# Optimization experiments

Measured on AMD Instinct MI355X. Metric: run time of the kernel, lower is better.

## Reference

```python
import jax, jax.numpy as jnp
import numpy as np

B, L, D, H = 2, 1024, 1024, 16
HD = D // H
HIDDEN = 4 * D
EPS = 1e-6
SCALE = HD ** -0.5

# RoPE tables (head_dim is even, so rope_dim == head_dim)
_inv_freq = 1.0 / (10000.0 ** (np.arange(0, HD, 2, dtype=np.float32) / HD))
_freqs = np.arange(L, dtype=np.float32)[:, None] * _inv_freq[None, :]          # [L, HD/2]
COS = jnp.asarray(np.concatenate([np.cos(_freqs), np.cos(_freqs)], -1))        # [L, HD]
SIN = jnp.asarray(np.concatenate([np.sin(_freqs), np.sin(_freqs)], -1))
MASK = jnp.tril(jnp.ones((L, L), dtype=bool))                                   # causal


def _clin(xr, xi, Wr, Wi, br=None, bi=None):
    # complex linear: (a+bi)(c+di), weights stored [out, in] as in torch
    r = xr @ Wr.T - xi @ Wi.T
    i = xr @ Wi.T + xi @ Wr.T
    if br is not None:
        r = r + br
        i = i + bi
    return r, i


def _cln(xr, xi, gr, gi, br, bi):
    mr = xr.mean(-1, keepdims=True)
    mi = xi.mean(-1, keepdims=True)
    cr = xr - mr
    ci = xi - mi
    var = (cr * cr + ci * ci).mean(-1, keepdims=True)
    s = jnp.sqrt(var + EPS)
    nr = cr / s
    ni = ci / s
    return nr * gr - ni * gi + br, nr * gi + ni * gr + bi


def _rot_half(x):
    h = x.shape[-1] // 2
    return jnp.concatenate([-x[..., h:], x[..., :h]], -1)


def _rope(xr, xi):
    # apply same real rotation to real and imag parts (matches torch code)
    return (xr * COS + _rot_half(xr) * SIN, xi * COS + _rot_half(xi) * SIN)


def _split_heads(x):
    return x.reshape(B, L, H, HD).transpose(0, 2, 1, 3)  # [B,H,L,HD]


def _merge_heads(x):
    return x.transpose(0, 2, 1, 3).reshape(B, L, D)


def setup_inputs() -> dict:
    key = jax.random.key(0)
    ks = jax.random.split(key, 20)
    n = lambda k, shape, s=1.0: jax.random.normal(k, shape, dtype=jnp.float32) * s
    s_attn = (2.0 * (D + D)) ** -0.5
    s_fc1 = (2.0 * (D + HIDDEN)) ** -0.5
    s_fc2 = (2.0 * (HIDDEN + D)) ** -0.5
    return {
        'x_real': n(ks[0], (B, L, D)),
        'x_imag': n(ks[1], (B, L, D)),
        'Wq_r': n(ks[2], (D, D), s_attn), 'Wq_i': n(ks[3], (D, D), s_attn),
        'Wk_r': n(ks[4], (D, D), s_attn), 'Wk_i': n(ks[5], (D, D), s_attn),
        'Wv_r': n(ks[6], (D, D), s_attn), 'Wv_i': n(ks[7], (D, D), s_attn),
        'Wo_r': n(ks[8], (D, D), s_attn), 'Wo_i': n(ks[9], (D, D), s_attn),
        'bo_r': jnp.zeros((D,), jnp.float32), 'bo_i': jnp.zeros((D,), jnp.float32),
        'ln1_gr': jnp.ones((D,), jnp.float32), 'ln1_gi': jnp.zeros((D,), jnp.float32),
        'ln1_br': jnp.zeros((D,), jnp.float32), 'ln1_bi': jnp.zeros((D,), jnp.float32),
        'ln2_gr': jnp.ones((D,), jnp.float32), 'ln2_gi': jnp.zeros((D,), jnp.float32),
        'ln2_br': jnp.zeros((D,), jnp.float32), 'ln2_bi': jnp.zeros((D,), jnp.float32),
        'W1_r': n(ks[10], (HIDDEN, D), s_fc1), 'W1_i': n(ks[11], (HIDDEN, D), s_fc1),
        'b1_r': jnp.zeros((HIDDEN,), jnp.float32), 'b1_i': jnp.zeros((HIDDEN,), jnp.float32),
        'W2_r': n(ks[12], (D, HIDDEN), s_fc2), 'W2_i': n(ks[13], (D, HIDDEN), s_fc2),
        'b2_r': jnp.zeros((D,), jnp.float32), 'b2_i': jnp.zeros((D,), jnp.float32),
        'mod_b': n(ks[14], (HIDDEN,), 0.1),
    }


def reference(x_real, x_imag,
              Wq_r, Wq_i, Wk_r, Wk_i, Wv_r, Wv_i, Wo_r, Wo_i, bo_r, bo_i,
              ln1_gr, ln1_gi, ln1_br, ln1_bi, ln2_gr, ln2_gi, ln2_br, ln2_bi,
              W1_r, W1_i, b1_r, b1_i, W2_r, W2_i, b2_r, b2_i, mod_b):
    # --- attention sublayer (pre-LN) ---
    hr, hi = _cln(x_real, x_imag, ln1_gr, ln1_gi, ln1_br, ln1_bi)
    Qr, Qi = _clin(hr, hi, Wq_r, Wq_i)
    Kr, Ki = _clin(hr, hi, Wk_r, Wk_i)
    Vr, Vi = _clin(hr, hi, Wv_r, Wv_i)
    Qr, Qi, Kr, Ki = map(_split_heads, (Qr, Qi, Kr, Ki))
    Vr, Vi = _split_heads(Vr), _split_heads(Vi)
    Qr, Qi = _rope(Qr, Qi)
    Kr, Ki = _rope(Kr, Ki)
    # Hermitian inner product real part: Re(Q K*) = Qr.Kr + Qi.Ki
    scores = (jnp.einsum('bhld,bhmd->bhlm', Qr, Kr)
              + jnp.einsum('bhld,bhmd->bhlm', Qi, Ki)) * SCALE
    scores = jnp.where(MASK, scores, -jnp.inf)
    attn = jax.nn.softmax(scores, axis=-1)
    out_r = _merge_heads(jnp.einsum('bhlm,bhmd->bhld', attn, Vr))
    out_i = _merge_heads(jnp.einsum('bhlm,bhmd->bhld', attn, Vi))
    out_r, out_i = _clin(out_r, out_i, Wo_r, Wo_i, bo_r, bo_i)
    ar = x_real + out_r
    ai = x_imag + out_i
    # --- feed-forward sublayer (pre-LN) ---
    hr, hi = _cln(ar, ai, ln2_gr, ln2_gi, ln2_br, ln2_bi)
    fr, fi = _clin(hr, hi, W1_r, W1_i, b1_r, b1_i)
    # ModReLU: relu(|z| + b) * e^{i angle(z)}
    mag = jnp.sqrt(fr * fr + fi * fi)
    safe = jnp.where(mag > 0, mag, 1.0)
    act = jax.nn.relu(mag + mod_b)
    fr, fi = act * fr / safe, act * fi / safe
    fr, fi = _clin(fr, fi, W2_r, W2_i, b2_r, b2_i)
    return ar + fr, ai + fi
```

## Files before the change

### kernel.cpp

```cpp
#include <hip/hip_runtime.h>

#define Bq 2
#define Lq 1024
#define Dq 1024
#define Hq 16
#define HDq 64
#define HIDq 4096
#define Mq (Bq*Lq)

typedef __bf16 bf16x8 __attribute__((ext_vector_type(8)));
typedef float floatx4 __attribute__((ext_vector_type(4)));
typedef float floatx16 __attribute__((ext_vector_type(16)));

__device__ __forceinline__ unsigned short f2us(float f){
  unsigned u = __builtin_bit_cast(unsigned, f);
  u = u + 0x7fffu + ((u >> 16) & 1u);
  return (unsigned short)(u >> 16);
}

__device__ __forceinline__ void gld16(const unsigned short* g, unsigned short* l){
  __builtin_amdgcn_global_load_lds(
      (const __attribute__((address_space(1))) unsigned int*)g,
      (__attribute__((address_space(3))) unsigned int*)l, 16, 0, 0);
}

__global__ __launch_bounds__(256) void cvt4_kernel(
    const float* __restrict__ s0, const float* __restrict__ s1,
    const float* __restrict__ s2, const float* __restrict__ s3,
    unsigned short* __restrict__ d0, unsigned short* __restrict__ d1,
    unsigned short* __restrict__ d2, unsigned short* __restrict__ d3,
    int n)
{
  const int a = blockIdx.y;
  const float* s = (a==0) ? s0 : (a==1) ? s1 : (a==2) ? s2 : s3;
  unsigned short* d = (a==0) ? d0 : (a==1) ? d1 : (a==2) ? d2 : d3;
  const int i = (blockIdx.x * 256 + threadIdx.x) * 8;
  if (i >= n) return;
  float4 v0 = ((const float4*)(s + i))[0];
  float4 v1 = ((const float4*)(s + i))[1];
  ushort4 o0, o1;
  o0.x=f2us(v0.x); o0.y=f2us(v0.y); o0.z=f2us(v0.z); o0.w=f2us(v0.w);
  o1.x=f2us(v1.x); o1.y=f2us(v1.y); o1.z=f2us(v1.z); o1.w=f2us(v1.w);
  ((ushort4*)(d + i))[0] = o0;
  ((ushort4*)(d + i))[1] = o1;
}

__global__ __launch_bounds__(256) void cln_kernel(
    const float* __restrict__ xr, const float* __restrict__ xi,
    const float* __restrict__ gr, const float* __restrict__ gi,
    const float* __restrict__ br, const float* __restrict__ bi,
    unsigned short* __restrict__ outr, unsigned short* __restrict__ outi)
{
  const int row = blockIdx.x;
  const int t = threadIdx.x;
  const int lane = t & 63, wv = t >> 6;
  __shared__ float sred[8];

  float4 v4r = ((const float4*)(xr + (size_t)row*Dq))[t];
  float4 v4i = ((const float4*)(xi + (size_t)row*Dq))[t];
  float vr[4] = {v4r.x, v4r.y, v4r.z, v4r.w};
  float vi[4] = {v4i.x, v4i.y, v4i.z, v4i.w};
  float sr = vr[0]+vr[1]+vr[2]+vr[3];
  float si = vi[0]+vi[1]+vi[2]+vi[3];
  #pragma unroll
  for (int o=32;o>0;o>>=1){ sr += __shfl_down(sr,o,64); si += __shfl_down(si,o,64); }
  if (lane==0){ sred[wv]=sr; sred[4+wv]=si; }
  __syncthreads();
  float mr = (sred[0]+sred[1]+sred[2]+sred[3]) * (1.0f/Dq);
  float mi = (sred[4]+sred[5]+sred[6]+sred[7]) * (1.0f/Dq);
  float cr[4], ci[4], vs = 0.f;
  #pragma unroll
  for (int j=0;j<4;++j){ cr[j]=vr[j]-mr; ci[j]=vi[j]-mi; vs += cr[j]*cr[j]+ci[j]*ci[j]; }
  #pragma unroll
  for (int o=32;o>0;o>>=1) vs += __shfl_down(vs,o,64);
  __syncthreads();
  if (lane==0) sred[wv]=vs;
  __syncthreads();
  float var = (sred[0]+sred[1]+sred[2]+sred[3]) * (1.0f/Dq);
  float inv = rsqrtf(var + 1e-6f);

  float4 g4r = ((const float4*)gr)[t];
  float4 g4i = ((const float4*)gi)[t];
  float4 b4r = ((const float4*)br)[t];
  float4 b4i = ((const float4*)bi)[t];
  float grf[4] = {g4r.x,g4r.y,g4r.z,g4r.w};
  float gif[4] = {g4i.x,g4i.y,g4i.z,g4i.w};
  float brf[4] = {b4r.x,b4r.y,b4r.z,b4r.w};
  float bif[4] = {b4i.x,b4i.y,b4i.z,b4i.w};
  ushort4 o_r, o_i;
  unsigned short orr[4], oii[4];
  #pragma unroll
  for (int j=0;j<4;++j){
    float nr = cr[j]*inv, ni = ci[j]*inv;
    orr[j] = f2us(nr*grf[j] - ni*gif[j] + brf[j]);
    oii[j] = f2us(nr*gif[j] + ni*grf[j] + bif[j]);
  }
  o_r.x=orr[0]; o_r.y=orr[1]; o_r.z=orr[2]; o_r.w=orr[3];
  o_i.x=oii[0]; o_i.y=oii[1]; o_i.z=oii[2]; o_i.w=oii[3];
  ((ushort4*)(outr + (size_t)row*Dq))[t] = o_r;
  ((ushort4*)(outi + (size_t)row*Dq))[t] = o_i;
}

template<int EPI, bool ROPE, bool SPLIT3>
__global__ __launch_bounds__(128,2) void cgemm32_kernel(
    const unsigned short* __restrict__ Ar, const unsigned short* __restrict__ Ai,
    const unsigned short* __restrict__ Wr, const unsigned short* __restrict__ Wi,
    void* __restrict__ Cr0, void* __restrict__ Ci0,
    void* __restrict__ Cr1, void* __restrict__ Ci1,
    void* __restrict__ Cr2, void* __restrict__ Ci2,
    const float* __restrict__ biasR, const float* __restrict__ biasI,
    const float* __restrict__ resR, const float* __restrict__ resI,
    const float* __restrict__ modb,
    int Ndim, int Kdim)
{
  const int t = threadIdx.x;
  const int w = t >> 6, l = t & 63;
  const int l31 = l & 31, lhi = l >> 5;
  const int m0 = blockIdx.x * 64, n0 = blockIdx.y * 64;

  __shared__ __align__(16) unsigned short sAr0[64*64], sAi0[64*64], sWr0[64*64], sWi0[64*64];
  __shared__ __align__(16) unsigned short sAr1[64*64], sAi1[64*64], sWr1[64*64], sWi1[64*64];

  floatx16 accRR[2], accII[2], accRI[2], accIR[2];
  #pragma unroll
  for (int i=0;i<2;++i){
    #pragma unroll
    for (int r=0;r<16;++r){ accRR[i][r]=0.f; accII[i][r]=0.f; accRI[i][r]=0.f; accIR[i][r]=0.f; }
  }

  const int srow = t >> 3;
  const int lc = (((t & 7) ^ ((t >> 3) & 7))) * 8;
  const unsigned short* pAr = Ar + (size_t)(m0 + srow)*Kdim + lc;
  const unsigned short* pAi = Ai + (size_t)(m0 + srow)*Kdim + lc;
  const unsigned short* pWr = Wr + (size_t)(n0 + srow)*Kdim + lc;
  const unsigned short* pWi = Wi + (size_t)(n0 + srow)*Kdim + lc;
  const int dst0 = t * 8;

  const int arow = w*32 + l31;
  int aoff[4], woff0[4], woff1[4];
  #pragma unroll
  for (int kh=0; kh<4; ++kh){
    const int c = kh*2 + lhi;
    aoff[kh]  = arow*64      + ((c ^ (arow & 7)) * 8);
    woff0[kh] = l31*64       + ((c ^ (l31 & 7)) * 8);
    woff1[kh] = (32+l31)*64  + ((c ^ (l31 & 7)) * 8);
  }

#define STAGEK(SA, SB, SC, SD, KOFF) do{                                   \
    _Pragma("unroll")                                                      \
    for (int j_=0;j_<4;++j_){                                              \
      const size_t so_ = (size_t)j_ * 16 * Kdim + (size_t)(KOFF);          \
      gld16(pAr + so_, &SA[dst0 + j_*1024]);                               \
      gld16(pAi + so_, &SB[dst0 + j_*1024]);                               \
      gld16(pWr + so_, &SC[dst0 + j_*1024]);                               \
      gld16(pWi + so_, &SD[dst0 + j_*1024]);                               \
    } }while(0)

#define COMPUTEK(SA, SB, SC, SD) do{                                       \
    _Pragma("unroll")                                                      \
    for (int kh_=0; kh_<4; ++kh_){                                         \
      bf16x8 fAr  = *(const bf16x8*)&SA[aoff[kh_]];                        \
      bf16x8 fAi  = *(const bf16x8*)&SB[aoff[kh_]];                        \
      bf16x8 fW0r = *(const bf16x8*)&SC[woff0[kh_]];                       \
      bf16x8 fW0i = *(const bf16x8*)&SD[woff0[kh_]];                       \
      bf16x8 fW1r = *(const bf16x8*)&SC[woff1[kh_]];                       \
      bf16x8 fW1i = *(const bf16x8*)&SD[woff1[kh_]];                       \
      accRR[0] = __builtin_amdgcn_mfma_f32_32x32x16_bf16(fAr, fW0r, accRR[0], 0,0,0); \
      accII[0] = __builtin_amdgcn_mfma_f32_32x32x16_bf16(fAi, fW0i, accII[0], 0,0,0); \
      accRI[0] = __builtin_amdgcn_mfma_f32_32x32x16_bf16(fAr, fW0i, accRI[0], 0,0,0); \
      accIR[0] = __builtin_amdgcn_mfma_f32_32x32x16_bf16(fAi, fW0r, accIR[0], 0,0,0); \
      accRR[1] = __builtin_amdgcn_mfma_f32_32x32x16_bf16(fAr, fW1r, accRR[1], 0,0,0); \
      accII[1] = __builtin_amdgcn_mfma_f32_32x32x16_bf16(fAi, fW1i, accII[1], 0,0,0); \
      accRI[1] = __builtin_amdgcn_mfma_f32_32x32x16_bf16(fAr, fW1i, accRI[1], 0,0,0); \
      accIR[1] = __builtin_amdgcn_mfma_f32_32x32x16_bf16(fAi, fW1r, accIR[1], 0,0,0); \
    } }while(0)

  const int nk = Kdim >> 6;
  STAGEK(sAr0, sAi0, sWr0, sWi0, 0);
  __syncthreads();
  for (int kk=0; kk<nk; kk+=2){
    STAGEK(sAr1, sAi1, sWr1, sWi1, (kk+1)*64);
    COMPUTEK(sAr0, sAi0, sWr0, sWi0);
    __syncthreads();
    if (kk+2 < nk) STAGEK(sAr0, sAi0, sWr0, sWi0, (kk+2)*64);
    COMPUTEK(sAr1, sAi1, sWr1, sWi1);
    __syncthreads();
  }
#undef STAGEK
#undef COMPUTEK

  float cr[2][16], ci[2][16];
  #pragma unroll
  for (int nf=0; nf<2; ++nf)
    #pragma unroll
    for (int r=0;r<16;++r){
      cr[nf][r] = accRR[nf][r] - accII[nf][r];
      ci[nf][r] = accRI[nf][r] + accIR[nf][r];
    }

  const bool doRope = ROPE && (!SPLIT3 || (n0 < 2048));
  if (doRope){
    const float invf = powf(10000.0f, -(float)l31 * (1.0f/32.0f));
    #pragma unroll
    for (int r=0;r<16;++r){
      const int gm = m0 + w*32 + (r&3) + 8*(r>>2) + 4*lhi;
      float s, c;
      sincosf((float)(gm & (Lq-1)) * invf, &s, &c);
      float xr_ = cr[0][r], yr_ = cr[1][r];
      cr[0][r] = xr_*c - yr_*s;  cr[1][r] = yr_*c + xr_*s;
      float xi_ = ci[0][r], yi_ = ci[1][r];
      ci[0][r] = xi_*c - yi_*s;  ci[1][r] = yi_*c + xi_*s;
    }
  }

  unsigned short *oR16 = nullptr, *oI16 = nullptr;
  float *oR32 = nullptr, *oI32 = nullptr;
  int ncol0, Nst;
  if (SPLIT3){
    const int aid = n0 >> 10;
    void* vr = (aid==0) ? Cr0 : ((aid==1) ? Cr1 : Cr2);
    void* vi = (aid==0) ? Ci0 : ((aid==1) ? Ci1 : Ci2);
    oR16 = (unsigned short*)vr; oI16 = (unsigned short*)vi;
    ncol0 = n0 & 1023; Nst = 1024;
  } else {
    oR16 = (unsigned short*)Cr0; oI16 = (unsigned short*)Ci0;
    oR32 = (float*)Cr0;          oI32 = (float*)Ci0;
    ncol0 = n0; Nst = Ndim;
  }

  #pragma unroll
  for (int nf=0; nf<2; ++nf){
    const int gn = n0 + nf*32 + l31;
    const int cn = ncol0 + nf*32 + l31;
    float bR = 0.f, bI = 0.f, mb = 0.f;
    if (EPI >= 1){ bR = biasR[gn]; bI = biasI[gn]; }
    if (EPI == 2){ mb = modb[gn]; }
    #pragma unroll
    for (int r=0;r<16;++r){
      const int gm = m0 + w*32 + (r&3) + 8*(r>>2) + 4*lhi;
      const size_t idx = (size_t)gm*Nst + cn;
      float vr_ = cr[nf][r] + bR, vi_ = ci[nf][r] + bI;
      if (EPI == 1 || EPI == 3){ vr_ += resR[idx]; vi_ += resI[idx]; }
      if (EPI == 2){
        float mag = sqrtf(vr_*vr_ + vi_*vi_);
        float safe = (mag > 0.f) ? mag : 1.0f;
        float act = fmaxf(mag + mb, 0.f);
        float sc = act / safe;
        vr_ *= sc; vi_ *= sc;
      }
      if (EPI == 0 || EPI == 2){
        oR16[idx] = f2us(vr_);
        oI16[idx] = f2us(vi_);
      } else {
        oR32[idx] = vr_;
        oI32[idx] = vi_;
      }
    }
  }
}

__global__ __launch_bounds__(256) void vtrans_kernel(
    const unsigned short* __restrict__ Vr, const unsigned short* __restrict__ Vi,
    unsigned short* __restrict__ VTr, unsigned short* __restrict__ VTi)
{
  const int lt = blockIdx.x;
  const int bh = blockIdx.y;
  const int h = bh & (Hq-1), b = bh >> 4;
  const int t = threadIdx.x;
  __shared__ unsigned short sTr[64*65], sTi[64*65];

  const int row = t >> 2;
  const int dc  = (t & 3) * 16;
  const size_t g = ((size_t)(b*Lq) + lt*64 + row)*Dq + h*HDq + dc;
  uint4 a0 = *(const uint4*)(Vr + g);
  uint4 a1 = *(const uint4*)(Vr + g + 8);
  uint4 b0 = *(const uint4*)(Vi + g);
  uint4 b1 = *(const uint4*)(Vi + g + 8);
  const unsigned short* pa0 = (const unsigned short*)&a0;
  const unsigned short* pa1 = (const unsigned short*)&a1;
  const unsigned short* pb0 = (const unsigned short*)&b0;
  const unsigned short* pb1 = (const unsigned short*)&b1;
  #pragma unroll
  for (int e=0;e<8;++e){
    sTr[(dc+e)*65 + row]   = pa0[e];
    sTr[(dc+8+e)*65 + row] = pa1[e];
    sTi[(dc+e)*65 + row]   = pb0[e];
    sTi[(dc+8+e)*65 + row] = pb1[e];
  }
  __syncthreads();
  const int d  = t >> 2;
  const int lcx = (t & 3) * 16;
  unsigned short bufr[16], bufi[16];
  #pragma unroll
  for (int e=0;e<16;++e){
    bufr[e] = sTr[d*65 + lcx + e];
    bufi[e] = sTi[d*65 + lcx + e];
  }
  const size_t og = ((size_t)bh*HDq + d)*Lq + lt*64 + lcx;
  *(uint4*)(VTr + og)     = *(const uint4*)&bufr[0];
  *(uint4*)(VTr + og + 8) = *(const uint4*)&bufr[8];
  *(uint4*)(VTi + og)     = *(const uint4*)&bufi[0];
  *(uint4*)(VTi + og + 8) = *(const uint4*)&bufi[8];
}

__device__ __forceinline__ int swz(int v){ return v ^ ((v >> 4) & 7); }

__global__ __launch_bounds__(256,2) void fattn_kernel(
    const unsigned short* __restrict__ Qr, const unsigned short* __restrict__ Qi,
    const unsigned short* __restrict__ Kr, const unsigned short* __restrict__ Ki,
    const unsigned short* __restrict__ VTr, const unsigned short* __restrict__ VTi,
    unsigned short* __restrict__ Or, unsigned short* __restrict__ Oi)
{
  const int qt = (int)(gridDim.x - 1 - blockIdx.x);
  const int bh = blockIdx.y;
  const int h = bh & (Hq-1), b = bh >> 4;
  const int t = threadIdx.x;
  const int w = t >> 6, lane = t & 63;
  const int quad = lane >> 4, l15 = lane & 15;

  __shared__ __align__(16) unsigned short sKr[4096], sKi[4096], sVr[4096], sVi[4096];
  __shared__ __align__(16) unsigned short sP[64*72];

  const size_t qbase = ((size_t)(b*Lq) + qt*64 + w*16 + l15)*Dq + h*HDq;
  bf16x8 qr_lo = *(const bf16x8*)(Qr + qbase + quad*8);
  bf16x8 qr_hi = *(const bf16x8*)(Qr + qbase + 32 + quad*8);
  bf16x8 qi_lo = *(const bf16x8*)(Qi + qbase + quad*8);
  bf16x8 qi_hi = *(const bf16x8*)(Qi + qbase + 32 + quad*8);

  const floatx4 fzero = {0.f,0.f,0.f,0.f};
  floatx4 aOr[4], aOi[4];
  #pragma unroll
  for (int i=0;i<4;++i){ aOr[i]=fzero; aOi[i]=fzero; }
  float m_run[4] = {-1e30f,-1e30f,-1e30f,-1e30f};
  float l_run[4] = {0.f,0.f,0.f,0.f};

  const int srow = t >> 2;
  const int sns  = srow >> 4;
  const int sl15 = srow & 15;
  const int q8   = (t & 3) * 2;
  const int dstA = sns*1024 + swz(q8*16 + sl15)*8;
  const int dstB = sns*1024 + swz((q8+1)*16 + sl15)*8;

  const int rd0 = swz(quad*16 + l15)*8;
  const int rd1 = swz((4+quad)*16 + l15)*8;

  for (int kt = 0; kt <= qt; ++kt){
    const size_t kg = ((size_t)(b*Lq) + kt*64 + srow)*Dq + h*HDq + q8*8;
    uint4 ka = *(const uint4*)(Kr + kg);
    uint4 kb = *(const uint4*)(Kr + kg + 8);
    uint4 kc = *(const uint4*)(Ki + kg);
    uint4 kd = *(const uint4*)(Ki + kg + 8);
    const size_t vg = ((size_t)bh*HDq + srow)*Lq + kt*64 + q8*8;
    uint4 va = *(const uint4*)(VTr + vg);
    uint4 vb = *(const uint4*)(VTr + vg + 8);
    uint4 vc = *(const uint4*)(VTi + vg);
    uint4 vd = *(const uint4*)(VTi + vg + 8);
    __syncthreads();
    *(uint4*)&sKr[dstA] = ka;  *(uint4*)&sKr[dstB] = kb;
    *(uint4*)&sKi[dstA] = kc;  *(uint4*)&sKi[dstB] = kd;
    *(uint4*)&sVr[dstA] = va;  *(uint4*)&sVr[dstB] = vb;
    *(uint4*)&sVi[dstA] = vc;  *(uint4*)&sVi[dstB] = vd;
    __syncthreads();

    floatx4 sc[4];
    #pragma unroll
    for (int ns=0; ns<4; ++ns){
      floatx4 x = fzero;
      x = __builtin_amdgcn_mfma_f32_16x16x32_bf16(qr_lo, *(const bf16x8*)&sKr[ns*1024 + rd0], x, 0,0,0);
      x = __builtin_amdgcn_mfma_f32_16x16x32_bf16(qr_hi, *(const bf16x8*)&sKr[ns*1024 + rd1], x, 0,0,0);
      x = __builtin_amdgcn_mfma_f32_16x16x32_bf16(qi_lo, *(const bf16x8*)&sKi[ns*1024 + rd0], x, 0,0,0);
      x = __builtin_amdgcn_mfma_f32_16x16x32_bf16(qi_hi, *(const bf16x8*)&sKi[ns*1024 + rd1], x, 0,0,0);
      sc[ns] = x;
    }

    const bool diag = (kt == qt);
    float rmax[4] = {-1e30f,-1e30f,-1e30f,-1e30f};
    #pragma unroll
    for (int ns=0; ns<4; ++ns){
      #pragma unroll
      for (int r=0; r<4; ++r){
        float s = sc[ns][r] * 0.125f;
        if (diag && (ns*16 + l15 > w*16 + quad*4 + r)) s = -1e30f;
        sc[ns][r] = s;
        rmax[r] = fmaxf(rmax[r], s);
      }
    }
    #pragma unroll
    for (int off=1; off<16; off<<=1){
      #pragma unroll
      for (int r=0; r<4; ++r) rmax[r] = fmaxf(rmax[r], __shfl_xor(rmax[r], off, 64));
    }

    float alpha[4], rsum[4];
    #pragma unroll
    for (int r=0; r<4; ++r){
      float mn = fmaxf(m_run[r], rmax[r]);
      alpha[r] = __expf(m_run[r] - mn);
      m_run[r] = mn;
      rsum[r] = 0.f;
    }
    #pragma unroll
    for (int ns=0; ns<4; ++ns){
      #pragma unroll
      for (int r=0; r<4; ++r){
        float p = __expf(sc[ns][r] - m_run[r]);
        rsum[r] += p;
        sP[(w*16 + quad*4 + r)*72 + ns*16 + l15] = f2us(p);
      }
    }
    #pragma unroll
    for (int off=1; off<16; off<<=1){
      #pragma unroll
      for (int r=0; r<4; ++r) rsum[r] += __shfl_xor(rsum[r], off, 64);
    }
    #pragma unroll
    for (int r=0; r<4; ++r) l_run[r] = l_run[r]*alpha[r] + rsum[r];
    #pragma unroll
    for (int ds=0; ds<4; ++ds)
      #pragma unroll
      for (int r=0; r<4; ++r){ aOr[ds][r] *= alpha[r]; aOi[ds][r] *= alpha[r]; }

    #pragma unroll
    for (int step=0; step<2; ++step){
      bf16x8 pf = *(const bf16x8*)&sP[(w*16 + l15)*72 + step*32 + quad*8];
      const int ro = (step==0) ? rd0 : rd1;
      #pragma unroll
      for (int ds=0; ds<4; ++ds){
        aOr[ds] = __builtin_amdgcn_mfma_f32_16x16x32_bf16(pf, *(const bf16x8*)&sVr[ds*1024 + ro], aOr[ds], 0,0,0);
        aOi[ds] = __builtin_amdgcn_mfma_f32_16x16x32_bf16(pf, *(const bf16x8*)&sVi[ds*1024 + ro], aOi[ds], 0,0,0);
      }
    }
  }

  #pragma unroll
  for (int r=0; r<4; ++r){
    const float il = 1.0f / l_run[r];
    const size_t ob = ((size_t)(b*Lq) + qt*64 + w*16 + quad*4 + r)*Dq + h*HDq;
    #pragma unroll
    for (int ds=0; ds<4; ++ds){
      Or[ob + ds*16 + l15] = f2us(aOr[ds][r] * il);
      Oi[ob + ds*16 + l15] = f2us(aOi[ds][r] * il);
    }
  }
}

extern "C" void kernel_launch(void* const* d_in, const int* in_sizes, int n_in,
                              void* d_out, int out_size, void* d_ws, size_t ws_size,
                              hipStream_t stream)
{
  const float* x_r    = (const float*)d_in[0];
  const float* x_i    = (const float*)d_in[1];
  const float* Wq_r   = (const float*)d_in[2];
  const float* Wq_i   = (const float*)d_in[3];
  const float* Wk_r   = (const float*)d_in[4];
  const float* Wk_i   = (const float*)d_in[5];
  const float* Wv_r   = (const float*)d_in[6];
  const float* Wv_i   = (const float*)d_in[7];
  const float* Wo_r   = (const float*)d_in[8];
  const float* Wo_i   = (const float*)d_in[9];
  const float* bo_r   = (const float*)d_in[10];
  const float* bo_i   = (const float*)d_in[11];
  const float* ln1_gr = (const float*)d_in[12];
  const float* ln1_gi = (const float*)d_in[13];
  const float* ln1_br = (const float*)d_in[14];
  const float* ln1_bi = (const float*)d_in[15];
  const float* ln2_gr = (const float*)d_in[16];
  const float* ln2_gi = (const float*)d_in[17];
  const float* ln2_br = (const float*)d_in[18];
  const float* ln2_bi = (const float*)d_in[19];
  const float* W1_r   = (const float*)d_in[20];
  const float* W1_i   = (const float*)d_in[21];
  const float* b1_r   = (const float*)d_in[22];
  const float* b1_i   = (const float*)d_in[23];
  const float* W2_r   = (const float*)d_in[24];
  const float* W2_i   = (const float*)d_in[25];
  const float* b2_r   = (const float*)d_in[26];
  const float* b2_i   = (const float*)d_in[27];
  const float* mod_b  = (const float*)d_in[28];

  char* wsb = (char*)d_ws;
  const size_t MB = 1024*1024;
  unsigned short* bQKV_r = (unsigned short*)(wsb + 0*MB);
  unsigned short* bQKV_i = (unsigned short*)(wsb + 6*MB);
  unsigned short* bWo_r = (unsigned short*)(wsb + 12*MB);
  unsigned short* bWo_i = (unsigned short*)(wsb + 14*MB);
  unsigned short* bW1_r = (unsigned short*)(wsb + 16*MB);
  unsigned short* bW1_i = (unsigned short*)(wsb + 24*MB);
  unsigned short* bW2_r = (unsigned short*)(wsb + 32*MB);
  unsigned short* bW2_i = (unsigned short*)(wsb + 40*MB);
  unsigned short* hr  = (unsigned short*)(wsb + 48*MB);
  unsigned short* hi_ = (unsigned short*)(wsb + 52*MB);
  unsigned short* Qr  = (unsigned short*)(wsb + 56*MB);
  unsigned short* Qi  = (unsigned short*)(wsb + 60*MB);
  unsigned short* Kr  = (unsigned short*)(wsb + 64*MB);
  unsigned short* Ki  = (unsigned short*)(wsb + 68*MB);
  unsigned short* Vr  = (unsigned short*)(wsb + 72*MB);
  unsigned short* Vi  = (unsigned short*)(wsb + 76*MB);
  unsigned short* VTr = (unsigned short*)(wsb + 80*MB);
  unsigned short* VTi = (unsigned short*)(wsb + 84*MB);
  unsigned short* Or  = hr;
  unsigned short* Oi  = hi_;
  unsigned short* h2r = Qr;
  unsigned short* h2i = Qi;
  unsigned short* fr  = (unsigned short*)(wsb + 64*MB);
  unsigned short* fi  = (unsigned short*)(wsb + 80*MB);

  float* outR = (float*)d_out;
  float* outI = outR + (size_t)Mq*Dq;

  const dim3 blk(256);
  const dim3 blk128(128);

  const int nDD = Dq*Dq;
  const int nDH = Dq*HIDq;
  cvt4_kernel<<<dim3(nDD/2048, 4), blk, 0, stream>>>(Wq_r, Wk_r, Wv_r, Wo_r,
      bQKV_r, bQKV_r + (size_t)nDD, bQKV_r + (size_t)2*nDD, bWo_r, nDD);
  cvt4_kernel<<<dim3(nDD/2048, 4), blk, 0, stream>>>(Wq_i, Wk_i, Wv_i, Wo_i,
      bQKV_i, bQKV_i + (size_t)nDD, bQKV_i + (size_t)2*nDD, bWo_i, nDD);
  cvt4_kernel<<<dim3(nDH/2048, 4), blk, 0, stream>>>(W1_r, W1_i, W2_r, W2_i,
      bW1_r, bW1_i, bW2_r, bW2_i, nDH);

  cln_kernel<<<Mq, blk, 0, stream>>>(x_r, x_i, ln1_gr, ln1_gi, ln1_br, ln1_bi, hr, hi_);
  cgemm32_kernel<0,true,true><<<dim3(Mq/64, 3072/64), blk128, 0, stream>>>(
      hr, hi_, bQKV_r, bQKV_i,
      Qr, Qi, Kr, Ki, Vr, Vi,
      nullptr, nullptr, nullptr, nullptr, nullptr, 3072, Dq);
  vtrans_kernel<<<dim3(16, 32), blk, 0, stream>>>(Vr, Vi, VTr, VTi);
  fattn_kernel<<<dim3(16, 32), blk, 0, stream>>>(Qr, Qi, Kr, Ki, VTr, VTi, Or, Oi);
  cgemm32_kernel<1,false,false><<<dim3(Mq/64, Dq/64), blk128, 0, stream>>>(
      Or, Oi, bWo_r, bWo_i, outR, outI, nullptr, nullptr, nullptr, nullptr,
      bo_r, bo_i, x_r, x_i, nullptr, Dq, Dq);
  cln_kernel<<<Mq, blk, 0, stream>>>(outR, outI, ln2_gr, ln2_gi, ln2_br, ln2_bi, h2r, h2i);
  cgemm32_kernel<2,false,false><<<dim3(Mq/64, HIDq/64), blk128, 0, stream>>>(
      h2r, h2i, bW1_r, bW1_i, fr, fi, nullptr, nullptr, nullptr, nullptr,
      b1_r, b1_i, nullptr, nullptr, mod_b, HIDq, Dq);
  cgemm32_kernel<3,false,false><<<dim3(Mq/64, Dq/64), blk128, 0, stream>>>(
      fr, fi, bW2_r, bW2_i, outR, outI, nullptr, nullptr, nullptr, nullptr,
      b2_r, b2_i, outR, outI, nullptr, Dq, HIDq);
}
```

Measured before the change: 507.1 us.

## Switch complex GEMM to 16x16x32 MFMA with 4 waves and BK=32

Rewrites the complex GEMM kernel to use 256 threads (4 waves in a 2x2 grid) with 16x16x32 bf16 MFMA tiles instead of 2 waves with 32x32x16 MFMA, and halves the K-step staged into LDS to 32. The LDS footprint drops and the launch bound rises to allow more resident blocks, aiming at better latency hiding and occupancy. The trade-off is more sync barriers per K and less operand reuse per wave, since each wave covers a 32x32 output tile instead of 32x64. RoPE and epilogue indexing are remapped to the new accumulator layout.

```diff
diff --git a/kernel.cpp b/kernel.cpp
--- a/kernel.cpp
+++ b/kernel.cpp
@@ -10,7 +10,6 @@
 
 typedef __bf16 bf16x8 __attribute__((ext_vector_type(8)));
 typedef float floatx4 __attribute__((ext_vector_type(4)));
-typedef float floatx16 __attribute__((ext_vector_type(16)));
 
 __device__ __forceinline__ unsigned short f2us(float f){
   unsigned u = __builtin_bit_cast(unsigned, f);
@@ -102,7 +101,7 @@
 }
 
 template<int EPI, bool ROPE, bool SPLIT3>
-__global__ __launch_bounds__(128,2) void cgemm32_kernel(
+__global__ __launch_bounds__(256,3) void cgemm16_kernel(
     const unsigned short* __restrict__ Ar, const unsigned short* __restrict__ Ai,
     const unsigned short* __restrict__ Wr, const unsigned short* __restrict__ Wi,
     void* __restrict__ Cr0, void* __restrict__ Ci0,
@@ -114,103 +113,110 @@
     int Ndim, int Kdim)
 {
   const int t = threadIdx.x;
-  const int w = t >> 6, l = t & 63;
-  const int l31 = l & 31, lhi = l >> 5;
+  const int w = t >> 6, lane = t & 63;
+  const int quad = lane >> 4, l15 = lane & 15;
+  const int wr = w >> 1, wc = w & 1;
   const int m0 = blockIdx.x * 64, n0 = blockIdx.y * 64;
 
-  __shared__ __align__(16) unsigned short sAr0[64*64], sAi0[64*64], sWr0[64*64], sWi0[64*64];
-  __shared__ __align__(16) unsigned short sAr1[64*64], sAi1[64*64], sWr1[64*64], sWi1[64*64];
-
-  floatx16 accRR[2], accII[2], accRI[2], accIR[2];
-  #pragma unroll
-  for (int i=0;i<2;++i){
-    #pragma unroll
-    for (int r=0;r<16;++r){ accRR[i][r]=0.f; accII[i][r]=0.f; accRI[i][r]=0.f; accIR[i][r]=0.f; }
-  }
-
-  const int srow = t >> 3;
-  const int lc = (((t & 7) ^ ((t >> 3) & 7))) * 8;
+  __shared__ __align__(16) unsigned short sAr0[64*32], sAi0[64*32], sWr0[64*32], sWi0[64*32];
+  __shared__ __align__(16) unsigned short sAr1[64*32], sAi1[64*32], sWr1[64*32], sWi1[64*32];
+
+  const floatx4 fz = {0.f,0.f,0.f,0.f};
+  floatx4 accRR[2][2], accII[2][2], accRI[2][2], accIR[2][2];
+  #pragma unroll
+  for (int i=0;i<2;++i)
+    #pragma unroll
+    for (int j=0;j<2;++j){ accRR[i][j]=fz; accII[i][j]=fz; accRI[i][j]=fz; accIR[i][j]=fz; }
+
+  const int srow = t >> 2;
+  const int lc = ((t & 3) ^ ((t >> 2) & 3)) * 8;
   const unsigned short* pAr = Ar + (size_t)(m0 + srow)*Kdim + lc;
   const unsigned short* pAi = Ai + (size_t)(m0 + srow)*Kdim + lc;
   const unsigned short* pWr = Wr + (size_t)(n0 + srow)*Kdim + lc;
   const unsigned short* pWi = Wi + (size_t)(n0 + srow)*Kdim + lc;
   const int dst0 = t * 8;
 
-  const int arow = w*32 + l31;
-  int aoff[4], woff0[4], woff1[4];
-  #pragma unroll
-  for (int kh=0; kh<4; ++kh){
-    const int c = kh*2 + lhi;
-    aoff[kh]  = arow*64      + ((c ^ (arow & 7)) * 8);
-    woff0[kh] = l31*64       + ((c ^ (l31 & 7)) * 8);
-    woff1[kh] = (32+l31)*64  + ((c ^ (l31 & 7)) * 8);
-  }
+  const int arow0 = wr*32 + l15,       arow1 = arow0 + 16;
+  const int wrow0 = wc*16 + l15,       wrow1 = wrow0 + 32;
+  const int aoff0 = arow0*32 + ((quad ^ (arow0 & 3))*8);
+  const int aoff1 = arow1*32 + ((quad ^ (arow1 & 3))*8);
+  const int woff0 = wrow0*32 + ((quad ^ (wrow0 & 3))*8);
+  const int woff1 = wrow1*32 + ((quad ^ (wrow1 & 3))*8);
 
 #define STAGEK(SA, SB, SC, SD, KOFF) do{                                   \
-    _Pragma("unroll")                                                      \
-    for (int j_=0;j_<4;++j_){                                              \
-      const size_t so_ = (size_t)j_ * 16 * Kdim + (size_t)(KOFF);          \
-      gld16(pAr + so_, &SA[dst0 + j_*1024]);                               \
-      gld16(pAi + so_, &SB[dst0 + j_*1024]);                               \
-      gld16(pWr + so_, &SC[dst0 + j_*1024]);                               \
-      gld16(pWi + so_, &SD[dst0 + j_*1024]);                               \
-    } }while(0)
+    gld16(pAr + (KOFF), &SA[dst0]);                                        \
+    gld16(pAi + (KOFF), &SB[dst0]);                                        \
+    gld16(pWr + (KOFF), &SC[dst0]);                                        \
+    gld16(pWi + (KOFF), &SD[dst0]);                                        \
+  }while(0)
 
 #define COMPUTEK(SA, SB, SC, SD) do{                                       \
-    _Pragma("unroll")                                                      \
-    for (int kh_=0; kh_<4; ++kh_){                                         \
-      bf16x8 fAr  = *(const bf16x8*)&SA[aoff[kh_]];                        \
-      bf16x8 fAi  = *(const bf16x8*)&SB[aoff[kh_]];                        \
-      bf16x8 fW0r = *(const bf16x8*)&SC[woff0[kh_]];                       \
-      bf16x8 fW0i = *(const bf16x8*)&SD[woff0[kh_]];                       \
-      bf16x8 fW1r = *(const bf16x8*)&SC[woff1[kh_]];                       \
-      bf16x8 fW1i = *(const bf16x8*)&SD[woff1[kh_]];                       \
-      accRR[0] = __builtin_amdgcn_mfma_f32_32x32x16_bf16(fAr, fW0r, accRR[0], 0,0,0); \
-      accII[0] = __builtin_amdgcn_mfma_f32_32x32x16_bf16(fAi, fW0i, accII[0], 0,0,0); \
-      accRI[0] = __builtin_amdgcn_mfma_f32_32x32x16_bf16(fAr, fW0i, accRI[0], 0,0,0); \
-      accIR[0] = __builtin_amdgcn_mfma_f32_32x32x16_bf16(fAi, fW0r, accIR[0], 0,0,0); \
-      accRR[1] = __builtin_amdgcn_mfma_f32_32x32x16_bf16(fAr, fW1r, accRR[1], 0,0,0); \
-      accII[1] = __builtin_amdgcn_mfma_f32_32x32x16_bf16(fAi, fW1i, accII[1], 0,0,0); \
-      accRI[1] = __builtin_amdgcn_mfma_f32_32x32x16_bf16(fAr, fW1i, accRI[1], 0,0,0); \
-      accIR[1] = __builtin_amdgcn_mfma_f32_32x32x16_bf16(fAi, fW1r, accIR[1], 0,0,0); \
-    } }while(0)
-
-  const int nk = Kdim >> 6;
+    bf16x8 fA0r = *(const bf16x8*)&SA[aoff0];                              \
+    bf16x8 fA1r = *(const bf16x8*)&SA[aoff1];                              \
+    bf16x8 fA0i = *(const bf16x8*)&SB[aoff0];                              \
+    bf16x8 fA1i = *(const bf16x8*)&SB[aoff1];                              \
+    bf16x8 fW0r = *(const bf16x8*)&SC[woff0];                              \
+    bf16x8 fW1r = *(const bf16x8*)&SC[woff1];                              \
+    bf16x8 fW0i = *(const bf16x8*)&SD[woff0];                              \
+    bf16x8 fW1i = *(const bf16x8*)&SD[woff1];                              \
+    accRR[0][0] = __builtin_amdgcn_mfma_f32_16x16x32_bf16(fA0r, fW0r, accRR[0][0], 0,0,0); \
+    accII[0][0] = __builtin_amdgcn_mfma_f32_16x16x32_bf16(fA0i, fW0i, accII[0][0], 0,0,0); \
+    accRI[0][0] = __builtin_amdgcn_mfma_f32_16x16x32_bf16(fA0r, fW0i, accRI[0][0], 0,0,0); \
+    accIR[0][0] = __builtin_amdgcn_mfma_f32_16x16x32_bf16(fA0i, fW0r, accIR[0][0], 0,0,0); \
+    accRR[0][1] = __builtin_amdgcn_mfma_f32_16x16x32_bf16(fA0r, fW1r, accRR[0][1], 0,0,0); \
+    accII[0][1] = __builtin_amdgcn_mfma_f32_16x16x32_bf16(fA0i, fW1i, accII[0][1], 0,0,0); \
+    accRI[0][1] = __builtin_amdgcn_mfma_f32_16x16x32_bf16(fA0r, fW1i, accRI[0][1], 0,0,0); \
+    accIR[0][1] = __builtin_amdgcn_mfma_f32_16x16x32_bf16(fA0i, fW1r, accIR[0][1], 0,0,0); \
+    accRR[1][0] = __builtin_amdgcn_mfma_f32_16x16x32_bf16(fA1r, fW0r, accRR[1][0], 0,0,0); \
+    accII[1][0] = __builtin_amdgcn_mfma_f32_16x16x32_bf16(fA1i, fW0i, accII[1][0], 0,0,0); \
+    accRI[1][0] = __builtin_amdgcn_mfma_f32_16x16x32_bf16(fA1r, fW0i, accRI[1][0], 0,0,0); \
+    accIR[1][0] = __builtin_amdgcn_mfma_f32_16x16x32_bf16(fA1i, fW0r, accIR[1][0], 0,0,0); \
+    accRR[1][1] = __builtin_amdgcn_mfma_f32_16x16x32_bf16(fA1r, fW1r, accRR[1][1], 0,0,0); \
+    accII[1][1] = __builtin_amdgcn_mfma_f32_16x16x32_bf16(fA1i, fW1i, accII[1][1], 0,0,0); \
+    accRI[1][1] = __builtin_amdgcn_mfma_f32_16x16x32_bf16(fA1r, fW1i, accRI[1][1], 0,0,0); \
+    accIR[1][1] = __builtin_amdgcn_mfma_f32_16x16x32_bf16(fA1i, fW1r, accIR[1][1], 0,0,0); \
+  }while(0)
+
+  const int nk = Kdim >> 5;
   STAGEK(sAr0, sAi0, sWr0, sWi0, 0);
   __syncthreads();
   for (int kk=0; kk<nk; kk+=2){
-    STAGEK(sAr1, sAi1, sWr1, sWi1, (kk+1)*64);
+    STAGEK(sAr1, sAi1, sWr1, sWi1, (size_t)(kk+1)*32);
     COMPUTEK(sAr0, sAi0, sWr0, sWi0);
     __syncthreads();
-    if (kk+2 < nk) STAGEK(sAr0, sAi0, sWr0, sWi0, (kk+2)*64);
+    if (kk+2 < nk) STAGEK(sAr0, sAi0, sWr0, sWi0, (size_t)(kk+2)*32);
     COMPUTEK(sAr1, sAi1, sWr1, sWi1);
     __syncthreads();
   }
 #undef STAGEK
 #undef COMPUTEK
 
-  float cr[2][16], ci[2][16];
-  #pragma unroll
-  for (int nf=0; nf<2; ++nf)
-    #pragma unroll
-    for (int r=0;r<16;++r){
-      cr[nf][r] = accRR[nf][r] - accII[nf][r];
-      ci[nf][r] = accRI[nf][r] + accIR[nf][r];
-    }
+  float cr[2][2][4], ci[2][2][4];
+  #pragma unroll
+  for (int mf=0; mf<2; ++mf)
+    #pragma unroll
+    for (int nf=0; nf<2; ++nf)
+      #pragma unroll
+      for (int r=0;r<4;++r){
+        cr[mf][nf][r] = accRR[mf][nf][r] - accII[mf][nf][r];
+        ci[mf][nf][r] = accRI[mf][nf][r] + accIR[mf][nf][r];
+      }
 
   const bool doRope = ROPE && (!SPLIT3 || (n0 < 2048));
   if (doRope){
-    const float invf = powf(10000.0f, -(float)l31 * (1.0f/32.0f));
-    #pragma unroll
-    for (int r=0;r<16;++r){
-      const int gm = m0 + w*32 + (r&3) + 8*(r>>2) + 4*lhi;
-      float s, c;
-      sincosf((float)(gm & (Lq-1)) * invf, &s, &c);
-      float xr_ = cr[0][r], yr_ = cr[1][r];
-      cr[0][r] = xr_*c - yr_*s;  cr[1][r] = yr_*c + xr_*s;
-      float xi_ = ci[0][r], yi_ = ci[1][r];
-      ci[0][r] = xi_*c - yi_*s;  ci[1][r] = yi_*c + xi_*s;
-    }
+    const float invf = powf(10000.0f, -(float)(wc*16 + l15) * (1.0f/32.0f));
+    #pragma unroll
+    for (int mf=0; mf<2; ++mf)
+      #pragma unroll
+      for (int r=0;r<4;++r){
+        const int gm = m0 + wr*32 + mf*16 + quad*4 + r;
+        float s, c;
+        sincosf((float)(gm & (Lq-1)) * invf, &s, &c);
+        float xr_ = cr[mf][0][r], yr_ = cr[mf][1][r];
+        cr[mf][0][r] = xr_*c - yr_*s;  cr[mf][1][r] = yr_*c + xr_*s;
+        float xi_ = ci[mf][0][r], yi_ = ci[mf][1][r];
+        ci[mf][0][r] = xi_*c - yi_*s;  ci[mf][1][r] = yi_*c + xi_*s;
+      }
   }
 
   unsigned short *oR16 = nullptr, *oI16 = nullptr;
@@ -230,32 +236,34 @@
 
   #pragma unroll
   for (int nf=0; nf<2; ++nf){
-    const int gn = n0 + nf*32 + l31;
-    const int cn = ncol0 + nf*32 + l31;
+    const int gn = n0 + wc*16 + nf*32 + l15;
+    const int cn = ncol0 + wc*16 + nf*32 + l15;
     float bR = 0.f, bI = 0.f, mb = 0.f;
     if (EPI >= 1){ bR = biasR[gn]; bI = biasI[gn]; }
     if (EPI == 2){ mb = modb[gn]; }
     #pragma unroll
-    for (int r=0;r<16;++r){
-      const int gm = m0 + w*32 + (r&3) + 8*(r>>2) + 4*lhi;
-      const size_t idx = (size_t)gm*Nst + cn;
-      float vr_ = cr[nf][r] + bR, vi_ = ci[nf][r] + bI;
-      if (EPI == 1 || EPI == 3){ vr_ += resR[idx]; vi_ += resI[idx]; }
-      if (EPI == 2){
-        float mag = sqrtf(vr_*vr_ + vi_*vi_);
-        float safe = (mag > 0.f) ? mag : 1.0f;
-        float act = fmaxf(mag + mb, 0.f);
-        float sc = act / safe;
-        vr_ *= sc; vi_ *= sc;
+    for (int mf=0; mf<2; ++mf)
+      #pragma unroll
+      for (int r=0;r<4;++r){
+        const int gm = m0 + wr*32 + mf*16 + quad*4 + r;
+        const size_t idx = (size_t)gm*Nst + cn;
+        float vr_ = cr[mf][nf][r] + bR, vi_ = ci[mf][nf][r] + bI;
+        if (EPI == 1 || EPI == 3){ vr_ += resR[idx]; vi_ += resI[idx]; }
+        if (EPI == 2){
+          float mag = sqrtf(vr_*vr_ + vi_*vi_);
+          float safe = (mag > 0.f) ? mag : 1.0f;
+          float act = fmaxf(mag + mb, 0.f);
+          float sc = act / safe;
+          vr_ *= sc; vi_ *= sc;
+        }
+        if (EPI == 0 || EPI == 2){
+          oR16[idx] = f2us(vr_);
+          oI16[idx] = f2us(vi_);
+        } else {
+          oR32[idx] = vr_;
+          oI32[idx] = vi_;
+        }
       }
-      if (EPI == 0 || EPI == 2){
-        oR16[idx] = f2us(vr_);
-        oI16[idx] = f2us(vi_);
-      } else {
-        oR32[idx] = vr_;
-        oI32[idx] = vi_;
-      }
-    }
   }
 }
 
@@ -509,7 +517,6 @@
   float* outI = outR + (size_t)Mq*Dq;
 
   const dim3 blk(256);
-  const dim3 blk128(128);
 
   const int nDD = Dq*Dq;
   const int nDH = Dq*HIDq;
@@ -521,20 +528,20 @@
       bW1_r, bW1_i, bW2_r, bW2_i, nDH);
 
   cln_kernel<<<Mq, blk, 0, stream>>>(x_r, x_i, ln1_gr, ln1_gi, ln1_br, ln1_bi, hr, hi_);
-  cgemm32_kernel<0,true,true><<<dim3(Mq/64, 3072/64), blk128, 0, stream>>>(
+  cgemm16_kernel<0,true,true><<<dim3(Mq/64, 3072/64), blk, 0, stream>>>(
       hr, hi_, bQKV_r, bQKV_i,
       Qr, Qi, Kr, Ki, Vr, Vi,
       nullptr, nullptr, nullptr, nullptr, nullptr, 3072, Dq);
   vtrans_kernel<<<dim3(16, 32), blk, 0, stream>>>(Vr, Vi, VTr, VTi);
   fattn_kernel<<<dim3(16, 32), blk, 0, stream>>>(Qr, Qi, Kr, Ki, VTr, VTi, Or, Oi);
-  cgemm32_kernel<1,false,false><<<dim3(Mq/64, Dq/64), blk128, 0, stream>>>(
+  cgemm16_kernel<1,false,false><<<dim3(Mq/64, Dq/64), blk, 0, stream>>>(
       Or, Oi, bWo_r, bWo_i, outR, outI, nullptr, nullptr, nullptr, nullptr,
       bo_r, bo_i, x_r, x_i, nullptr, Dq, Dq);
   cln_kernel<<<Mq, blk, 0, stream>>>(outR, outI, ln2_gr, ln2_gi, ln2_br, ln2_bi, h2r, h2i);
-  cgemm32_kernel<2,false,false><<<dim3(Mq/64, HIDq/64), blk128, 0, stream>>>(
+  cgemm16_kernel<2,false,false><<<dim3(Mq/64, HIDq/64), blk, 0, stream>>>(
       h2r, h2i, bW1_r, bW1_i, fr, fi, nullptr, nullptr, nullptr, nullptr,
       b1_r, b1_i, nullptr, nullptr, mod_b, HIDq, Dq);
-  cgemm32_kernel<3,false,false><<<dim3(Mq/64, Dq/64), blk128, 0, stream>>>(
+  cgemm16_kernel<3,false,false><<<dim3(Mq/64, Dq/64), blk, 0, stream>>>(
       fr, fi, bW2_r, bW2_i, outR, outI, nullptr, nullptr, nullptr, nullptr,
       b2_r, b2_i, outR, outI, nullptr, Dq, HIDq);
 }
```

After: 522.4 us. +3.0%, slower.

## Widen complex GEMM tile to 64x128 with four waves and K-step 32

Applied to the files above, without the earlier changes.

The complex GEMM block grows from 128 threads on a 64x64 output tile to 256 threads on a 64x128 tile. Each wave is placed on a 2x2 grid inside the block, and the K step per stage shrinks from 64 to 32. The shared-memory layout packs two rows per 64-element line with a new XOR swizzle. The goal is more A-tile reuse across N and more waves per block for latency hiding, at the cost of twice as many barriers per K and half as many blocks in each grid.

```diff
diff --git a/kernel.cpp b/kernel.cpp
--- a/kernel.cpp
+++ b/kernel.cpp
@@ -102,7 +102,7 @@
 }
 
 template<int EPI, bool ROPE, bool SPLIT3>
-__global__ __launch_bounds__(128,2) void cgemm32_kernel(
+__global__ __launch_bounds__(256,2) void cgemm_kernel(
     const unsigned short* __restrict__ Ar, const unsigned short* __restrict__ Ai,
     const unsigned short* __restrict__ Wr, const unsigned short* __restrict__ Wi,
     void* __restrict__ Cr0, void* __restrict__ Ci0,
@@ -116,10 +116,11 @@
   const int t = threadIdx.x;
   const int w = t >> 6, l = t & 63;
   const int l31 = l & 31, lhi = l >> 5;
-  const int m0 = blockIdx.x * 64, n0 = blockIdx.y * 64;
-
-  __shared__ __align__(16) unsigned short sAr0[64*64], sAi0[64*64], sWr0[64*64], sWi0[64*64];
-  __shared__ __align__(16) unsigned short sAr1[64*64], sAi1[64*64], sWr1[64*64], sWi1[64*64];
+  const int wm = w >> 1, wn = w & 1;
+  const int m0 = blockIdx.x * 64, n0 = blockIdx.y * 128;
+
+  __shared__ __align__(16) unsigned short sAr0[2048], sAi0[2048], sWr0[4096], sWi0[4096];
+  __shared__ __align__(16) unsigned short sAr1[2048], sAi1[2048], sWr1[4096], sWi1[4096];
 
   floatx16 accRR[2], accII[2], accRI[2], accIR[2];
   #pragma unroll
@@ -128,43 +129,53 @@
     for (int r=0;r<16;++r){ accRR[i][r]=0.f; accII[i][r]=0.f; accRI[i][r]=0.f; accIR[i][r]=0.f; }
   }
 
-  const int srow = t >> 3;
-  const int lc = (((t & 7) ^ ((t >> 3) & 7))) * 8;
-  const unsigned short* pAr = Ar + (size_t)(m0 + srow)*Kdim + lc;
-  const unsigned short* pAi = Ai + (size_t)(m0 + srow)*Kdim + lc;
-  const unsigned short* pWr = Wr + (size_t)(n0 + srow)*Kdim + lc;
-  const unsigned short* pWi = Wi + (size_t)(n0 + srow)*Kdim + lc;
-  const int dst0 = t * 8;
-
-  const int arow = w*32 + l31;
-  int aoff[4], woff0[4], woff1[4];
-  #pragma unroll
-  for (int kh=0; kh<4; ++kh){
-    const int c = kh*2 + lhi;
-    aoff[kh]  = arow*64      + ((c ^ (arow & 7)) * 8);
-    woff0[kh] = l31*64       + ((c ^ (l31 & 7)) * 8);
-    woff1[kh] = (32+l31)*64  + ((c ^ (l31 & 7)) * 8);
+  const int lnA = t >> 3, cpA = t & 7;
+  const int clA = cpA ^ (lnA & 7);
+  const int rwA = lnA*2 + (clA >> 2), kcA = clA & 3;
+  const unsigned short* pAr = Ar + (size_t)(m0 + rwA)*Kdim + kcA*8;
+  const unsigned short* pAi = Ai + (size_t)(m0 + rwA)*Kdim + kcA*8;
+  const int dA = t*8;
+  const int ln1 = (t+256) >> 3, cp1 = t & 7;
+  const int cl1 = cp1 ^ (ln1 & 7);
+  const int rw1 = ln1*2 + (cl1 >> 2), kc1 = cl1 & 3;
+  const unsigned short* pWr0 = Wr + (size_t)(n0 + rwA)*Kdim + kcA*8;
+  const unsigned short* pWi0 = Wi + (size_t)(n0 + rwA)*Kdim + kcA*8;
+  const unsigned short* pWr1 = Wr + (size_t)(n0 + rw1)*Kdim + kc1*8;
+  const unsigned short* pWi1 = Wi + (size_t)(n0 + rw1)*Kdim + kc1*8;
+  const int dW1 = (t+256)*8;
+
+  const int rA = wm*32 + l31;
+  const int lnRA = rA >> 1, bA = (rA & 1)*4;
+  int aoff[2];
+  #pragma unroll
+  for (int s=0;s<2;++s) aoff[s] = lnRA*64 + (((bA + s*2 + lhi) ^ (lnRA & 7)) * 8);
+  const int rW0 = wn*64 + l31,      lnW0 = rW0 >> 1, bW0 = (rW0 & 1)*4;
+  const int rW1 = wn*64 + 32 + l31, lnW1 = rW1 >> 1, bW1 = (rW1 & 1)*4;
+  int woff0[2], woff1[2];
+  #pragma unroll
+  for (int s=0;s<2;++s){
+    woff0[s] = lnW0*64 + (((bW0 + s*2 + lhi) ^ (lnW0 & 7)) * 8);
+    woff1[s] = lnW1*64 + (((bW1 + s*2 + lhi) ^ (lnW1 & 7)) * 8);
   }
 
 #define STAGEK(SA, SB, SC, SD, KOFF) do{                                   \
-    _Pragma("unroll")                                                      \
-    for (int j_=0;j_<4;++j_){                                              \
-      const size_t so_ = (size_t)j_ * 16 * Kdim + (size_t)(KOFF);          \
-      gld16(pAr + so_, &SA[dst0 + j_*1024]);                               \
-      gld16(pAi + so_, &SB[dst0 + j_*1024]);                               \
-      gld16(pWr + so_, &SC[dst0 + j_*1024]);                               \
-      gld16(pWi + so_, &SD[dst0 + j_*1024]);                               \
-    } }while(0)
+    gld16(pAr  + (KOFF), &SA[dA]);                                         \
+    gld16(pAi  + (KOFF), &SB[dA]);                                         \
+    gld16(pWr0 + (KOFF), &SC[dA]);                                         \
+    gld16(pWi0 + (KOFF), &SD[dA]);                                         \
+    gld16(pWr1 + (KOFF), &SC[dW1]);                                        \
+    gld16(pWi1 + (KOFF), &SD[dW1]);                                        \
+  }while(0)
 
 #define COMPUTEK(SA, SB, SC, SD) do{                                       \
     _Pragma("unroll")                                                      \
-    for (int kh_=0; kh_<4; ++kh_){                                         \
-      bf16x8 fAr  = *(const bf16x8*)&SA[aoff[kh_]];                        \
-      bf16x8 fAi  = *(const bf16x8*)&SB[aoff[kh_]];                        \
-      bf16x8 fW0r = *(const bf16x8*)&SC[woff0[kh_]];                       \
-      bf16x8 fW0i = *(const bf16x8*)&SD[woff0[kh_]];                       \
-      bf16x8 fW1r = *(const bf16x8*)&SC[woff1[kh_]];                       \
-      bf16x8 fW1i = *(const bf16x8*)&SD[woff1[kh_]];                       \
+    for (int s_=0; s_<2; ++s_){                                            \
+      bf16x8 fAr  = *(const bf16x8*)&SA[aoff[s_]];                         \
+      bf16x8 fAi  = *(const bf16x8*)&SB[aoff[s_]];                         \
+      bf16x8 fW0r = *(const bf16x8*)&SC[woff0[s_]];                        \
+      bf16x8 fW0i = *(const bf16x8*)&SD[woff0[s_]];                        \
+      bf16x8 fW1r = *(const bf16x8*)&SC[woff1[s_]];                        \
+      bf16x8 fW1i = *(const bf16x8*)&SD[woff1[s_]];                        \
       accRR[0] = __builtin_amdgcn_mfma_f32_32x32x16_bf16(fAr, fW0r, accRR[0], 0,0,0); \
       accII[0] = __builtin_amdgcn_mfma_f32_32x32x16_bf16(fAi, fW0i, accII[0], 0,0,0); \
       accRI[0] = __builtin_amdgcn_mfma_f32_32x32x16_bf16(fAr, fW0i, accRI[0], 0,0,0); \
@@ -175,14 +186,14 @@
       accIR[1] = __builtin_amdgcn_mfma_f32_32x32x16_bf16(fAi, fW1r, accIR[1], 0,0,0); \
     } }while(0)
 
-  const int nk = Kdim >> 6;
+  const int nk = Kdim >> 5;
   STAGEK(sAr0, sAi0, sWr0, sWi0, 0);
   __syncthreads();
   for (int kk=0; kk<nk; kk+=2){
-    STAGEK(sAr1, sAi1, sWr1, sWi1, (kk+1)*64);
+    STAGEK(sAr1, sAi1, sWr1, sWi1, (size_t)(kk+1)*32);
     COMPUTEK(sAr0, sAi0, sWr0, sWi0);
     __syncthreads();
-    if (kk+2 < nk) STAGEK(sAr0, sAi0, sWr0, sWi0, (kk+2)*64);
+    if (kk+2 < nk) STAGEK(sAr0, sAi0, sWr0, sWi0, (size_t)(kk+2)*32);
     COMPUTEK(sAr1, sAi1, sWr1, sWi1);
     __syncthreads();
   }
@@ -203,7 +214,7 @@
     const float invf = powf(10000.0f, -(float)l31 * (1.0f/32.0f));
     #pragma unroll
     for (int r=0;r<16;++r){
-      const int gm = m0 + w*32 + (r&3) + 8*(r>>2) + 4*lhi;
+      const int gm = m0 + wm*32 + (r&3) + 8*(r>>2) + 4*lhi;
       float s, c;
       sincosf((float)(gm & (Lq-1)) * invf, &s, &c);
       float xr_ = cr[0][r], yr_ = cr[1][r];
@@ -230,14 +241,14 @@
 
   #pragma unroll
   for (int nf=0; nf<2; ++nf){
-    const int gn = n0 + nf*32 + l31;
-    const int cn = ncol0 + nf*32 + l31;
+    const int gn = n0 + wn*64 + nf*32 + l31;
+    const int cn = ncol0 + wn*64 + nf*32 + l31;
     float bR = 0.f, bI = 0.f, mb = 0.f;
     if (EPI >= 1){ bR = biasR[gn]; bI = biasI[gn]; }
     if (EPI == 2){ mb = modb[gn]; }
     #pragma unroll
     for (int r=0;r<16;++r){
-      const int gm = m0 + w*32 + (r&3) + 8*(r>>2) + 4*lhi;
+      const int gm = m0 + wm*32 + (r&3) + 8*(r>>2) + 4*lhi;
       const size_t idx = (size_t)gm*Nst + cn;
       float vr_ = cr[nf][r] + bR, vi_ = ci[nf][r] + bI;
       if (EPI == 1 || EPI == 3){ vr_ += resR[idx]; vi_ += resI[idx]; }
@@ -509,7 +520,6 @@
   float* outI = outR + (size_t)Mq*Dq;
 
   const dim3 blk(256);
-  const dim3 blk128(128);
 
   const int nDD = Dq*Dq;
   const int nDH = Dq*HIDq;
@@ -521,20 +531,20 @@
       bW1_r, bW1_i, bW2_r, bW2_i, nDH);
 
   cln_kernel<<<Mq, blk, 0, stream>>>(x_r, x_i, ln1_gr, ln1_gi, ln1_br, ln1_bi, hr, hi_);
-  cgemm32_kernel<0,true,true><<<dim3(Mq/64, 3072/64), blk128, 0, stream>>>(
+  cgemm_kernel<0,true,true><<<dim3(Mq/64, 3072/128), blk, 0, stream>>>(
       hr, hi_, bQKV_r, bQKV_i,
       Qr, Qi, Kr, Ki, Vr, Vi,
       nullptr, nullptr, nullptr, nullptr, nullptr, 3072, Dq);
   vtrans_kernel<<<dim3(16, 32), blk, 0, stream>>>(Vr, Vi, VTr, VTi);
   fattn_kernel<<<dim3(16, 32), blk, 0, stream>>>(Qr, Qi, Kr, Ki, VTr, VTi, Or, Oi);
-  cgemm32_kernel<1,false,false><<<dim3(Mq/64, Dq/64), blk128, 0, stream>>>(
+  cgemm_kernel<1,false,false><<<dim3(Mq/64, Dq/128), blk, 0, stream>>>(
       Or, Oi, bWo_r, bWo_i, outR, outI, nullptr, nullptr, nullptr, nullptr,
       bo_r, bo_i, x_r, x_i, nullptr, Dq, Dq);
   cln_kernel<<<Mq, blk, 0, stream>>>(outR, outI, ln2_gr, ln2_gi, ln2_br, ln2_bi, h2r, h2i);
-  cgemm32_kernel<2,false,false><<<dim3(Mq/64, HIDq/64), blk128, 0, stream>>>(
+  cgemm_kernel<2,false,false><<<dim3(Mq/64, HIDq/128), blk, 0, stream>>>(
       h2r, h2i, bW1_r, bW1_i, fr, fi, nullptr, nullptr, nullptr, nullptr,
       b1_r, b1_i, nullptr, nullptr, mod_b, HIDq, Dq);
-  cgemm32_kernel<3,false,false><<<dim3(Mq/64, Dq/64), blk128, 0, stream>>>(
+  cgemm_kernel<3,false,false><<<dim3(Mq/64, Dq/128), blk, 0, stream>>>(
       fr, fi, bW2_r, bW2_i, outR, outI, nullptr, nullptr, nullptr, nullptr,
       b2_r, b2_i, outR, outI, nullptr, Dq, HIDq);
 }
```

New measurement: 530.5 us. 1.05x slower.
